# Optimization experiments

Hardware: AMD Instinct MI355X
Metric: run time of the kernel (lower is better)

## Reference

```python
import jax, jax.numpy as jnp
import numpy as np

EPS = 1e-3  # matches eps=0.001 in __init__


def p2o(psf, H, W):
    """PSF -> OTF: zero-pad to (H,W), roll so kernel center is at origin, FFT2."""
    B, C, kh, kw = psf.shape
    otf = jnp.zeros((B, C, H, W), psf.dtype).at[:, :, :kh, :kw].set(psf)
    otf = jnp.roll(otf, (-(kh // 2), -(kw // 2)), axis=(-2, -1))
    return jnp.fft.fft2(otf)


def splits_mean(a, sf):
    """Mean over the sf*sf distinct blocks of splits(): contiguous-chunk split
    via view(sf, H/sf, sf, W/sf); mean over the two sf axes equals mean over
    the scale^2 trailing dim of the original splits output."""
    B, C, H, W = a.shape
    return a.reshape(B, C, sf, H // sf, sf, W // sf).mean(axis=(2, 4))


def setup_inputs() -> dict:
    key = jax.random.key(0)
    kx, kk = jax.random.split(key)
    x = jax.random.normal(kx, (4, 64, 128, 128), dtype=jnp.float32)
    k = jax.random.uniform(kk, (4, 64, 25, 25), dtype=jnp.float32)
    alpha = jnp.zeros((1, 64, 1, 1), dtype=jnp.float32)  # learned parameter
    return {"x": x, "k": k, "alpha": alpha, "sf": 2}


def reference(x, k, alpha, sf):
    biaseps = jax.nn.sigmoid(alpha - 9.0) + EPS          # (1,C,1,1)
    B, C, h, w = x.shape
    H, W = h * sf, w * sf
    # s-fold zero-fill upsample (STy)
    STy = jnp.zeros((B, C, H, W), x.dtype).at[:, :, ::sf, ::sf].set(x)
    # nearest-neighbor interpolate by sf
    xu = jnp.repeat(jnp.repeat(x, sf, axis=-2), sf, axis=-1) if sf != 1 else x
    FB = p2o(k, H, W)                                    # complex (B,C,H,W)
    FBC = jnp.conj(FB)
    F2B = jnp.abs(FB) ** 2
    FBFy = FBC * jnp.fft.fft2(STy)
    FR = FBFy + jnp.fft.fft2(biaseps * xu)
    FBR = splits_mean(FB * FR, sf)                       # (B,C,H/sf,W/sf)
    invW = splits_mean(F2B, sf)
    invWBR = FBR / (invW + biaseps)
    FCBinvWBR = FBC * jnp.tile(invWBR, (1, 1, sf, sf))   # repeat(1,1,sf,sf)
    FX = (FR - FCBinvWBR) / biaseps
    return jnp.real(jnp.fft.ifft2(FX))
```

## Files before the change

kernel.cpp:

```cpp
#include <hip/hip_runtime.h>
#include <math.h>


static __device__ __forceinline__ float2 cmul(float2 a, float2 b) {
    return make_float2(a.x * b.x - a.y * b.y, a.x * b.y + a.y * b.x);
}
static __device__ __forceinline__ float2 cadd(float2 a, float2 b) {
    return make_float2(a.x + b.x, a.y + b.y);
}
static __device__ __forceinline__ float2 csub(float2 a, float2 b) {
    return make_float2(a.x - b.x, a.y - b.y);
}
static __device__ __forceinline__ float2 conjf2(float2 a) {
    return make_float2(a.x, -a.y);
}
static __device__ __forceinline__ int PHI(int i) { return i + (i >> 3); }

template <int HB, int SIGN, int THREADS>
static __device__ __forceinline__ void fill_tw(float2* tw) {
    for (int i = threadIdx.x; i < HB; i += THREADS) {
        float s, c;
        __sincosf((float)SIGN * (float)M_PI * (float)i / (float)HB, &s, &c);
        tw[i] = make_float2(c, s);
    }
}

template <int N, int R, int SIGN>
static __device__ __forceinline__ int fft_lds_rows(float2 (&buf)[2][R][N],
                                                   const float2* __restrict__ tw) {
    constexpr int HB = N / 2;
    const int tid = threadIdx.x;
    const int row = tid / HB;
    const int bt = tid % HB;
    int cur = 0, m = 1;
    for (int l = HB; l >= 1; l >>= 1) {
        __syncthreads();
        const int k = bt & (m - 1);
        const float2 w = tw[bt - k];
        float2 a = buf[cur][row][bt];
        float2 b = buf[cur][row][bt + HB];
        float2 d = make_float2(a.x - b.x, a.y - b.y);
        float2 wd = make_float2(w.x * d.x - w.y * d.y, w.x * d.y + w.y * d.x);
        const int o = 2 * bt - k;
        buf[cur ^ 1][row][o] = make_float2(a.x + b.x, a.y + b.y);
        buf[cur ^ 1][row][o + m] = wd;
        cur ^= 1;
        m <<= 1;
    }
    __syncthreads();
    return cur;
}

template <int SIGN, int NCOL>
static __device__ __forceinline__ int fft4_cols_wavelocal(float2 (&buf)[2][NCOL][130],
                                                          const float2* __restrict__ tw) {
    const int lane = threadIdx.x & 63;
    const int wv = threadIdx.x >> 6;
    const int col = wv * 4 + (lane >> 4);
    const int r = lane & 15;
    int cur = 0, m = 1;
#pragma unroll
    for (int st = 0; st < 3; ++st) {
#pragma unroll
        for (int b = 0; b < 2; ++b) {
            const int bq = r + 16 * b;
            const int k = bq & (m - 1);
            const int jm = bq - k;
            const float2 w1 = tw[jm];
            const float2 w2 = tw[2 * jm];
            const float2 w3 = tw[3 * jm];
            float2 a0 = buf[cur][col][bq];
            float2 a1 = buf[cur][col][bq + 32];
            float2 a2 = buf[cur][col][bq + 64];
            float2 a3 = buf[cur][col][bq + 96];
            float2 s02 = cadd(a0, a2), d02 = csub(a0, a2);
            float2 s13 = cadd(a1, a3), d13 = csub(a1, a3);
            float2 b0 = cadd(s02, s13), b2 = csub(s02, s13);
            float2 b1 = make_float2(d02.x - (float)SIGN * d13.y,
                                    d02.y + (float)SIGN * d13.x);
            float2 b3 = make_float2(d02.x + (float)SIGN * d13.y,
                                    d02.y - (float)SIGN * d13.x);
            const int o = 4 * jm + k;
            buf[cur ^ 1][col][o] = b0;
            buf[cur ^ 1][col][o + m] = cmul(w1, b1);
            buf[cur ^ 1][col][o + 2 * m] = cmul(w2, b2);
            buf[cur ^ 1][col][o + 3 * m] = cmul(w3, b3);
        }
        cur ^= 1;
        m <<= 2;
    }
#pragma unroll
    for (int b = 0; b < 4; ++b) {
        const int bt = r + 16 * b;
        float2 a = buf[cur][col][bt];
        float2 bb = buf[cur][col][bt + 64];
        buf[cur ^ 1][col][bt] = cadd(a, bb);
        buf[cur ^ 1][col][bt + 64] = csub(a, bb);
    }
    return cur ^ 1;
}

__global__ __launch_bounds__(256) void k1_fft_rows_x(const float* __restrict__ x,
                                                     float2* __restrict__ Fx) {
    __shared__ float2 buf[2][4][128];
    __shared__ float2 tw64m[64];
    const int tid = threadIdx.x;
    const int row = tid >> 6;
    const int t = tid & 63;
    fill_tw<64, -1, 256>(tw64m);
    const int gpair = blockIdx.x * 4 + row;
    const float* r0 = x + (size_t)gpair * 256;
    const float* r1 = r0 + 128;
    const float2 a0 = ((const float2*)r0)[t];
    const float2 a1 = ((const float2*)r1)[t];
    buf[0][row][2 * t].x = a0.x;
    buf[0][row][2 * t].y = a1.x;
    buf[0][row][2 * t + 1].x = a0.y;
    buf[0][row][2 * t + 1].y = a1.y;
    int cur = fft_lds_rows<128, 4, -1>(buf, tw64m);
    float2* d0 = Fx + (size_t)gpair * 256;
    float2* d1 = d0 + 128;
    for (int h = 0; h < 2; ++h) {
        int tt = t + h * 64;
        if (tt > 64) continue;
        float2 Zt = buf[cur][row][tt];
        float2 Zm = buf[cur][row][(128 - tt) & 127];
        d0[tt] = make_float2(0.5f * (Zt.x + Zm.x), 0.5f * (Zt.y - Zm.y));
        float ax = Zt.x - Zm.x, ay = Zt.y + Zm.y;
        d1[tt] = make_float2(0.5f * ay, -0.5f * ax);
    }
}

__global__ __launch_bounds__(256) void k2_fft_cols_x(float2* __restrict__ Fx) {
    __shared__ float2 buf[2][16][130];
    __shared__ float2 tw[96];
    const int tid = threadIdx.x;
    const int img = blockIdx.x / 5;
    const int c0 = (blockIdx.x % 5) * 16;
    for (int i = tid; i < 96; i += 256) {
        float s, c;
        __sincosf(-(float)M_PI * (float)i / 64.f, &s, &c);
        tw[i] = make_float2(c, s);
    }
    float2* base = Fx + (size_t)img * 16384 + c0;
    for (int it = 0; it < 8; ++it) {
        int idx = it * 256 + tid;
        int rr = idx >> 4, cc = idx & 15;
        buf[0][cc][rr] = base[rr * 128 + cc];
    }
    __syncthreads();
    int cur = fft4_cols_wavelocal<-1, 16>(buf, tw);
    __syncthreads();
    for (int it = 0; it < 8; ++it) {
        int idx = it * 256 + tid;
        int rr = idx >> 4, cc = idx & 15;
        base[rr * 128 + cc] = buf[cur][cc][rr];
    }
}

__global__ __launch_bounds__(128) void k3_fft_rows_k(const float* __restrict__ kin,
                                                     float2* __restrict__ FBtmp) {
    __shared__ float2 buf[2][1][256];
    __shared__ float2 tw128m[128];
    const int tid = threadIdx.x;
    const int img = blockIdx.x / 25;
    const int lr = blockIdx.x % 25;
    fill_tw<128, -1, 128>(tw128m);
    const float* krow = kin + img * 625 + lr * 25;
    for (int h = 0; h < 2; ++h) {
        int v = tid + h * 128;
        int pc = (v + 12) & 255;
        buf[0][0][v] = make_float2(pc < 25 ? krow[pc] : 0.f, 0.f);
    }
    int cur = fft_lds_rows<256, 1, -1>(buf, tw128m);
    float2* dst = FBtmp + (size_t)img * 6400 + lr * 256;
    dst[tid] = buf[cur][0][tid];
    dst[tid + 128] = buf[cur][0][tid + 128];
}

__global__ __launch_bounds__(256) void k4_dft_cols_k(const float2* __restrict__ FBtmp,
                                                     float2* __restrict__ FBh) {
    __shared__ float2 T[33][28];
    const int j = threadIdx.x;
    const int img = blockIdx.x >> 2;
    const int q = blockIdx.x & 3;
    const int ubeg = q * 33;
    const int nu = (ubeg + 33 < 129) ? 33 : (129 - ubeg);
    const float k2pi = -2.f * (float)M_PI / 256.f;

    for (int idx = j; idx < nu * 25; idx += 256) {
        const int ul = idx / 25;
        const int p = idx - ul * 25;
        const int u = ubeg + ul;
        float s, c;
        __sincosf(k2pi * (float)((u * (p + 244)) & 255), &s, &c);
        T[ul][p] = make_float2(c, s);
    }

    const float2* src = FBtmp + (size_t)img * 6400 + j;
    float2 S[25];
#pragma unroll
    for (int p = 0; p < 25; ++p) S[p] = src[p * 256];
    __syncthreads();

    float2* dst = FBh + (size_t)img * 33024 + j;
    for (int ul = 0; ul < nu; ++ul) {
        float2 a0 = make_float2(0.f, 0.f);
        float2 a1 = make_float2(0.f, 0.f);
#pragma unroll
        for (int p = 0; p < 25; ++p) {
            const float2 t = T[ul][p];
            const float2 s = S[p];
            if (p & 1) {
                a1.x = fmaf(t.x, s.x, fmaf(-t.y, s.y, a1.x));
                a1.y = fmaf(t.x, s.y, fmaf(t.y, s.x, a1.y));
            } else {
                a0.x = fmaf(t.x, s.x, fmaf(-t.y, s.y, a0.x));
                a0.y = fmaf(t.x, s.y, fmaf(t.y, s.x, a0.y));
            }
        }
        dst[(size_t)(ubeg + ul) * 256] = make_float2(a0.x + a1.x, a0.y + a1.y);
    }
}

__global__ __launch_bounds__(256) void k6_fused(const float2* __restrict__ FBh,
                                                const float2* __restrict__ Fx,
                                                const float* __restrict__ alpha,
                                                float2* __restrict__ Zf) {
    __shared__ float2 stage[4][256];
    __shared__ float2 buf[2][4][288];
    __shared__ float2 tw[192];
    const int tid = threadIdx.x;
    const int rs = tid >> 6;
    const int q = tid & 63;
    const int img = blockIdx.x / 33;
    const int bq = blockIdx.x % 33;
    const int pa = 2 * bq;
    const int pb = (pa + 1 < 65) ? (pa + 1) : 64;
    for (int i = tid; i < 192; i += 256) {
        float s, c;
        __sincosf((float)M_PI * (float)i / 128.f, &s, &c);
        tw[i] = make_float2(c, s);
    }
    {
        const float2* base = FBh + (size_t)img * 33024;
        stage[0][tid] = base[pa * 256 + tid];
        stage[1][tid] = base[(128 - pa) * 256 + tid];
        stage[2][tid] = base[pb * 256 + tid];
        stage[3][tid] = base[(128 - pb) * 256 + tid];
    }
    __syncthreads();

    const int p = (rs < 2) ? pa : pb;
    const int sb = rs & 2;
    const int u = ((rs & 1) == 0) ? p : (128 - p);
    const int um = u & 127;
    const int msel = (um == p) ? 0 : 1;
    const int mi = sb | msel;
    const int oi = sb | (1 - msel);

    const float ci = tw[um].x, si = -tw[um].y;
    const float b = 1.f / (1.f + __expf(9.f - alpha[img & 63])) + 1e-3f;
    const float scale = 1.f / 65536.f;
    const float2 Di0 = make_float2(1.f + ci, si);
    const float2 Di1 = make_float2(1.f - ci, -si);
    const float2 Du = (u < 128) ? Di0 : Di1;
#pragma unroll
    for (int h = 0; h < 2; ++h) {
        const int t = q + 64 * h;
        float2 f00 = stage[mi][t];
        float2 f01 = stage[mi][t + 128];
        float2 f10, f11;
        if (um == 0) {
            f10 = stage[oi][t];
            f11 = stage[oi][t + 128];
        } else {
            f10 = conjf2(stage[oi][(256 - t) & 255]);
            f11 = conjf2(stage[oi][128 - t]);
        }
        const bool mir = (t > 64);
        const int rr = mir ? ((128 - um) & 127) : um;
        const int cc = mir ? (128 - t) : t;
        float2 fx = Fx[(size_t)img * 16384 + rr * 128 + cc];
        if (mir) fx.y = -fx.y;
        const float cj = tw[t].x, sj = -tw[t].y;
        float2 Dj0 = make_float2(1.f + cj, sj);
        float2 Dj1 = make_float2(1.f - cj, -sj);
        float2 A = cadd(cmul(f00, Dj0), cmul(f01, Dj1));
        float2 Bt = cadd(cmul(f10, Dj0), cmul(f11, Dj1));
        float2 S1 = cadd(cmul(A, Di0), cmul(Bt, Di1));
        S1.x *= 0.25f;
        S1.y *= 0.25f;
        float S2 = 0.25f * (f00.x * f00.x + f00.y * f00.y + f01.x * f01.x + f01.y * f01.y +
                            f10.x * f10.x + f10.y * f10.y + f11.x * f11.x + f11.y * f11.y);
        float inv = 1.f / (S2 + b);
        float2 mm = make_float2((1.f - S1.x) * inv, (-S1.y) * inv);
        float2 c0v = (u < 128) ? f00 : f10;
        float2 c1v = (u < 128) ? f01 : f11;
        float2 t0 = cadd(cmul(conjf2(c0v), mm), cmul(Du, Dj0));
        float2 t1 = cadd(cmul(conjf2(c1v), mm), cmul(Du, Dj1));
        float2 FX0 = cmul(fx, t0);
        float2 FX1 = cmul(fx, t1);
        buf[0][rs][PHI(t)] = make_float2(FX0.x * scale, FX0.y * scale);
        buf[0][rs][PHI(t + 128)] = make_float2(FX1.x * scale, FX1.y * scale);
    }

    int cur = 0, m = 1;
#pragma unroll
    for (int st = 0; st < 4; ++st) {
        const int k = q & (m - 1);
        const int jm = q - k;
        const float2 w1 = tw[jm];
        const float2 w2 = tw[2 * jm];
        const float2 w3 = tw[3 * jm];
        float2 a0 = buf[cur][rs][PHI(q)];
        float2 a1 = buf[cur][rs][PHI(q + 64)];
        float2 a2 = buf[cur][rs][PHI(q + 128)];
        float2 a3 = buf[cur][rs][PHI(q + 192)];
        float2 s02 = cadd(a0, a2), d02 = csub(a0, a2);
        float2 s13 = cadd(a1, a3), d13 = csub(a1, a3);
        float2 b0 = cadd(s02, s13), b2v = csub(s02, s13);
        float2 b1 = make_float2(d02.x - d13.y, d02.y + d13.x);
        float2 b3 = make_float2(d02.x + d13.y, d02.y - d13.x);
        const int o = 4 * jm + k;
        buf[cur ^ 1][rs][PHI(o)] = b0;
        buf[cur ^ 1][rs][PHI(o + m)] = cmul(w1, b1);
        buf[cur ^ 1][rs][PHI(o + 2 * m)] = cmul(w2, b2v);
        buf[cur ^ 1][rs][PHI(o + 3 * m)] = cmul(w3, b3);
        cur ^= 1;
        m <<= 2;
    }
    __syncthreads();

    const int u0 = u;
    bool dowrite = ((rs & 1) == 0) ? true : (p > 0 && p < 64);
    if (pb == pa && rs >= 2) dowrite = false;
    if (dowrite) {
        const float2 w = tw[u0];
        float2* zb = Zf + (size_t)img * 32768 + (size_t)u0 * 256;
#pragma unroll
        for (int hh = 0; hh < 4; ++hh) {
            const int jj = q + 64 * hh;
            float2 su = buf[cur][rs][PHI(jj)];
            float2 s2 = buf[cur][rs ^ 1][PHI(jj)];
            float2 e = make_float2(su.x + s2.x, su.y - s2.y);
            float2 o_ = make_float2(su.x - s2.x, su.y + s2.y);
            float2 wo = cmul(w, o_);
            zb[jj] = make_float2(e.x - wo.y, e.y + wo.x);
        }
    }
}

__global__ __launch_bounds__(256) void k7_c2r(const float2* __restrict__ Zf,
                                              float* __restrict__ out) {
    __shared__ float2 buf[2][16][130];
    __shared__ float2 tw[96];
    const int tid = threadIdx.x;
    const int img = blockIdx.x >> 4;
    const int c0 = (blockIdx.x & 15) * 16;
    for (int i = tid; i < 96; i += 256) {
        float s, c;
        __sincosf((float)M_PI * (float)i / 64.f, &s, &c);
        tw[i] = make_float2(c, s);
    }
    const float2* zb = Zf + (size_t)img * 32768 + c0;
    for (int it = 0; it < 8; ++it) {
        int idx = it * 256 + tid;
        int rr = idx >> 4, cc = idx & 15;
        buf[0][cc][rr] = zb[rr * 256 + cc];
    }
    __syncthreads();
    int cur = fft4_cols_wavelocal<1, 16>(buf, tw);
    __syncthreads();
    float* ob = out + (size_t)img * 65536 + c0;
    for (int it = 0; it < 8; ++it) {
        int idx = it * 256 + tid;
        int n = idx >> 4, c = idx & 15;
        float2 y = buf[cur][c][n];
        ob[(2 * n) * 256 + c] = y.x;
        ob[(2 * n + 1) * 256 + c] = y.y;
    }
}

extern "C" void kernel_launch(void* const* d_in, const int* in_sizes, int n_in,
                              void* d_out, int out_size, void* d_ws, size_t ws_size,
                              hipStream_t stream) {
    const float* x = (const float*)d_in[0];
    const float* k = (const float*)d_in[1];
    const float* alpha = (const float*)d_in[2];
    float* out = (float*)d_out;

    float2* Fx = (float2*)d_ws;
    float2* FBh = Fx + 256 * 16384;
    float2* Zf = FBh + 256 * 33024;
    float2* FBtmp = Zf + 256 * 32768;

    hipLaunchKernelGGL(k1_fft_rows_x, dim3(4096), dim3(256), 0, stream, x, Fx);
    hipLaunchKernelGGL(k2_fft_cols_x, dim3(256 * 5), dim3(256), 0, stream, Fx);
    hipLaunchKernelGGL(k3_fft_rows_k, dim3(6400), dim3(128), 0, stream, k, FBtmp);
    hipLaunchKernelGGL(k4_dft_cols_k, dim3(1024), dim3(256), 0, stream, FBtmp, FBh);
    hipLaunchKernelGGL(k6_fused, dim3(256 * 33), dim3(256), 0, stream, FBh, Fx, alpha, Zf);
    hipLaunchKernelGGL(k7_c2r, dim3(4096), dim3(256), 0, stream, Zf, out);
}
```

Measured before the change: 190.5 us.

## Fuse kernel column DFT into k6 and drop FBh intermediate buffer

Removes the separate k4 column-DFT kernel and computes the needed PSF-spectrum rows (u and 128-u) inside k6 directly from the row-FFT output, using the symmetry that row 128-u shares twiddles with u up to a sign alternation. This eliminates a kernel launch and the write and read of the large FBh intermediate. In exchange, each k6 block reloads 25 rows of FBtmp per image and redoes 25-tap DFT work that k4 computed once, so redundant compute and reads grow by the number of blocks per image.

```diff
diff --git a/kernel.cpp b/kernel.cpp
--- a/kernel.cpp
+++ b/kernel.cpp
@@ -178,58 +178,14 @@
     dst[tid + 128] = buf[cur][0][tid + 128];
 }
 
-__global__ __launch_bounds__(256) void k4_dft_cols_k(const float2* __restrict__ FBtmp,
-                                                     float2* __restrict__ FBh) {
-    __shared__ float2 T[33][28];
-    const int j = threadIdx.x;
-    const int img = blockIdx.x >> 2;
-    const int q = blockIdx.x & 3;
-    const int ubeg = q * 33;
-    const int nu = (ubeg + 33 < 129) ? 33 : (129 - ubeg);
-    const float k2pi = -2.f * (float)M_PI / 256.f;
-
-    for (int idx = j; idx < nu * 25; idx += 256) {
-        const int ul = idx / 25;
-        const int p = idx - ul * 25;
-        const int u = ubeg + ul;
-        float s, c;
-        __sincosf(k2pi * (float)((u * (p + 244)) & 255), &s, &c);
-        T[ul][p] = make_float2(c, s);
-    }
-
-    const float2* src = FBtmp + (size_t)img * 6400 + j;
-    float2 S[25];
-#pragma unroll
-    for (int p = 0; p < 25; ++p) S[p] = src[p * 256];
-    __syncthreads();
-
-    float2* dst = FBh + (size_t)img * 33024 + j;
-    for (int ul = 0; ul < nu; ++ul) {
-        float2 a0 = make_float2(0.f, 0.f);
-        float2 a1 = make_float2(0.f, 0.f);
-#pragma unroll
-        for (int p = 0; p < 25; ++p) {
-            const float2 t = T[ul][p];
-            const float2 s = S[p];
-            if (p & 1) {
-                a1.x = fmaf(t.x, s.x, fmaf(-t.y, s.y, a1.x));
-                a1.y = fmaf(t.x, s.y, fmaf(t.y, s.x, a1.y));
-            } else {
-                a0.x = fmaf(t.x, s.x, fmaf(-t.y, s.y, a0.x));
-                a0.y = fmaf(t.x, s.y, fmaf(t.y, s.x, a0.y));
-            }
-        }
-        dst[(size_t)(ubeg + ul) * 256] = make_float2(a0.x + a1.x, a0.y + a1.y);
-    }
-}
-
-__global__ __launch_bounds__(256) void k6_fused(const float2* __restrict__ FBh,
+__global__ __launch_bounds__(256) void k6_fused(const float2* __restrict__ FBtmp,
                                                 const float2* __restrict__ Fx,
                                                 const float* __restrict__ alpha,
                                                 float2* __restrict__ Zf) {
     __shared__ float2 stage[4][256];
     __shared__ float2 buf[2][4][288];
     __shared__ float2 tw[192];
+    __shared__ float2 Tt[2][25];
     const int tid = threadIdx.x;
     const int rs = tid >> 6;
     const int q = tid & 63;
@@ -237,17 +193,64 @@
     const int bq = blockIdx.x % 33;
     const int pa = 2 * bq;
     const int pb = (pa + 1 < 65) ? (pa + 1) : 64;
+
+    const float2* src = FBtmp + (size_t)img * 6400 + tid;
+    float2 S[25];
+#pragma unroll
+    for (int p = 0; p < 25; ++p) S[p] = src[p * 256];
+
     for (int i = tid; i < 192; i += 256) {
         float s, c;
         __sincosf((float)M_PI * (float)i / 128.f, &s, &c);
         tw[i] = make_float2(c, s);
     }
     {
-        const float2* base = FBh + (size_t)img * 33024;
-        stage[0][tid] = base[pa * 256 + tid];
-        stage[1][tid] = base[(128 - pa) * 256 + tid];
-        stage[2][tid] = base[pb * 256 + tid];
-        stage[3][tid] = base[(128 - pb) * 256 + tid];
+        const float k2pi = -2.f * (float)M_PI / 256.f;
+        for (int i = tid; i < 50; i += 256) {
+            const int which = i / 25, p = i - which * 25;
+            const int u = which ? pb : pa;
+            float s, c;
+            __sincosf(k2pi * (float)((u * (p + 244)) & 255), &s, &c);
+            Tt[which][p] = make_float2(c, s);
+        }
+    }
+    __syncthreads();
+
+    {
+        float2 aA = make_float2(0.f, 0.f), bA = make_float2(0.f, 0.f);
+        float2 aB = make_float2(0.f, 0.f), bB = make_float2(0.f, 0.f);
+#pragma unroll
+        for (int p = 0; p < 25; ++p) {
+            const float2 s = S[p];
+            const float2 ta = Tt[0][p];
+            const float axx = ta.x * s.x, ayy = ta.y * s.y;
+            const float axy = ta.x * s.y, ayx = ta.y * s.x;
+            aA.x += axx - ayy;
+            aA.y += axy + ayx;
+            if (p & 1) {
+                bA.x -= axx + ayy;
+                bA.y -= axy - ayx;
+            } else {
+                bA.x += axx + ayy;
+                bA.y += axy - ayx;
+            }
+            const float2 tb = Tt[1][p];
+            const float bxx = tb.x * s.x, byy = tb.y * s.y;
+            const float bxy = tb.x * s.y, byx = tb.y * s.x;
+            aB.x += bxx - byy;
+            aB.y += bxy + byx;
+            if (p & 1) {
+                bB.x -= bxx + byy;
+                bB.y -= bxy - byx;
+            } else {
+                bB.x += bxx + byy;
+                bB.y += bxy - byx;
+            }
+        }
+        stage[0][tid] = aA;
+        stage[1][tid] = bA;
+        stage[2][tid] = aB;
+        stage[3][tid] = bB;
     }
     __syncthreads();
 
@@ -391,14 +394,12 @@
     float* out = (float*)d_out;
 
     float2* Fx = (float2*)d_ws;
-    float2* FBh = Fx + 256 * 16384;
-    float2* Zf = FBh + 256 * 33024;
+    float2* Zf = Fx + 256 * 16384;
     float2* FBtmp = Zf + 256 * 32768;
 
     hipLaunchKernelGGL(k1_fft_rows_x, dim3(4096), dim3(256), 0, stream, x, Fx);
     hipLaunchKernelGGL(k2_fft_cols_x, dim3(256 * 5), dim3(256), 0, stream, Fx);
     hipLaunchKernelGGL(k3_fft_rows_k, dim3(6400), dim3(128), 0, stream, k, FBtmp);
-    hipLaunchKernelGGL(k4_dft_cols_k, dim3(1024), dim3(256), 0, stream, FBtmp, FBh);
-    hipLaunchKernelGGL(k6_fused, dim3(256 * 33), dim3(256), 0, stream, FBh, Fx, alpha, Zf);
+    hipLaunchKernelGGL(k6_fused, dim3(256 * 33), dim3(256), 0, stream, FBtmp, Fx, alpha, Zf);
     hipLaunchKernelGGL(k7_c2r, dim3(4096), dim3(256), 0, stream, Zf, out);
 }
```

After: 185.1 us. 2.8% less time.
